# Kernel tuning notes

Measured on AMD Instinct MI355X. Metric: run time of the kernel, lower is better.

Reference implementation:

```python
import jax, jax.numpy as jnp
import numpy as np

N_HEADS = 4
DIM_K = 64
DIM_V = 64
D_MODEL = 256


def setup_inputs() -> dict:
    key = jax.random.key(0)
    ks = jax.random.split(key, 10)
    B, S = 8, 1024
    s = 1.0 / np.sqrt(D_MODEL)
    return {
        "x": jax.random.normal(ks[0], (B, S, D_MODEL), jnp.float32),
        "y": jax.random.normal(ks[1], (B, S, D_MODEL), jnp.float32),
        "Wq": jax.random.normal(ks[2], (D_MODEL, DIM_K * N_HEADS), jnp.float32) * s,
        "bq": jnp.zeros((DIM_K * N_HEADS,), jnp.float32),
        "Wk": jax.random.normal(ks[3], (D_MODEL, DIM_K * N_HEADS), jnp.float32) * s,
        "bk": jnp.zeros((DIM_K * N_HEADS,), jnp.float32),
        "Wv": jax.random.normal(ks[4], (D_MODEL, DIM_V * N_HEADS), jnp.float32) * s,
        "bv": jnp.zeros((DIM_V * N_HEADS,), jnp.float32),
        "Wo": jax.random.normal(ks[5], (DIM_V * N_HEADS, D_MODEL), jnp.float32) * s,
        "bo": jnp.zeros((D_MODEL,), jnp.float32),
    }


def reference(x, y, Wq, bq, Wk, bk, Wv, bv, Wo, bo):
    B, Sx, _ = x.shape
    Sy = y.shape[1]
    dk = DIM_K // N_HEADS  # head dim for Q/K (16)
    dv = DIM_V // N_HEADS  # head dim for V (16)
    # Faithful to the original reshape: leading dim becomes n_heads^2 pseudo-heads.
    Q = (x @ Wq + bq).reshape(-1, B, Sx, dk)   # [H2, B, Sx, dk]
    K = (y @ Wk + bk).reshape(-1, B, Sy, dk)   # [H2, B, Sy, dk]
    V = (y @ Wv + bv).reshape(-1, B, Sy, dv)   # [H2, B, Sy, dv]
    scale = 1.0 / np.sqrt(DIM_K)
    scores = jnp.einsum("hbqd,hbkd->hbqk", Q, K) * scale  # [H2, B, Sx, Sy]
    # Per-row lower median (torch.median semantics: lower of two middle values).
    n = scores.shape[-1]
    med = jnp.sort(scores, axis=-1)[..., (n - 1) // 2][..., None]
    # Mask out entries not strictly greater than the row median.
    scores = jnp.where(scores - med > 0, scores, -jnp.inf)
    probs = jax.nn.softmax(scores, axis=-1)
    out = jnp.einsum("hbqk,hbkd->hbqd", probs, V)          # [H2, B, Sx, dv]
    out = jnp.transpose(out, (0, 2, 1, 3)).reshape(B, Sx, -1)  # [B, Sx, H2*dv]
    return out @ Wo + bo
```

## Files before the change

kernel.cpp:

```cpp
#include <hip/hip_runtime.h>
#include <stdint.h>


typedef _Float16 f16x8 __attribute__((ext_vector_type(8)));
typedef _Float16 f16x4 __attribute__((ext_vector_type(4)));
typedef float    f32x4 __attribute__((ext_vector_type(4)));

__global__ __launch_bounds__(256) void prepW(
    const float* __restrict__ Wq, const float* __restrict__ Wk,
    const float* __restrict__ Wv, const float* __restrict__ Wo,
    _Float16* __restrict__ P)
{
    __shared__ float T[64][65];
    const int mat = blockIdx.y;
    const float* W = (mat == 0) ? Wq : (mat == 1) ? Wk : (mat == 2) ? Wv : Wo;
    const int tk = blockIdx.x >> 2, tn = blockIdx.x & 3;
    const int t  = threadIdx.x;
    const int cl = t & 63, rg = t >> 6;

    #pragma unroll
    for (int r = 0; r < 16; ++r) {
        const int k = (rg << 4) + r;
        T[k][cl] = W[(size_t)((tk << 6) + k) * 256 + (tn << 6) + cl];
    }
    __syncthreads();
    _Float16* hi = P + ((size_t)mat << 17);
    _Float16* lo = hi + 65536;
    #pragma unroll
    for (int r = 0; r < 16; ++r) {
        const int n = (rg << 4) + r;
        const float v = T[cl][n];
        const _Float16 h = (_Float16)v;
        const size_t o = (size_t)((tn << 6) + n) * 256 + (tk << 6) + cl;
        hi[o] = h;
        lo[o] = (_Float16)(v - (float)h);
    }
}

__device__ __forceinline__ void gemm_mfma(const float* __restrict__ A,
                                          const _Float16* __restrict__ Whi,
                                          const _Float16* __restrict__ Wlo,
                                          const float* __restrict__ bias,
                                          float* __restrict__ C, int vf16)
{
    __shared__ _Float16 Bhi[64][136];
    __shared__ _Float16 Blo[64][136];
    const int tid = threadIdx.x;
    const int m0 = blockIdx.x << 7, n0 = blockIdx.y << 6;

    const int wv = tid >> 6, lane = tid & 63;
    const int fm = lane & 15, fq = lane >> 4;
    const int arow = m0 + (wv << 4) + fm;
    const float* abase = A + (size_t)arow * 256;

    const int srow = tid >> 4;
    const int skl  = (tid & 15) << 3;

    f32x4 acc[4];
    #pragma unroll
    for (int cb = 0; cb < 4; ++cb) { acc[cb][0]=0.f; acc[cb][1]=0.f; acc[cb][2]=0.f; acc[cb][3]=0.f; }

    float4 a0 = *(const float4*)(abase + (fq << 3));
    float4 a1 = *(const float4*)(abase + (fq << 3) + 4);

    #pragma unroll
    for (int h = 0; h < 2; ++h) {
        if (h) __syncthreads();
        #pragma unroll
        for (int p = 0; p < 2; ++p) {
            const int n = (p << 5) + srow;
            const size_t off = (size_t)(n0 + n) * 256 + (h << 7) + skl;
            *(f16x8*)&Bhi[n][skl] = *(const f16x8*)(Whi + off);
            *(f16x8*)&Blo[n][skl] = *(const f16x8*)(Wlo + off);
        }
        __syncthreads();

        #pragma unroll
        for (int kb = 0; kb < 4; ++kb) {
            const int ks = (h << 2) + kb;
            float4 n0v = a0, n1v = a1;
            if (ks < 7) {
                const float* np = abase + ((ks + 1) << 5) + (fq << 3);
                n0v = *(const float4*)np;
                n1v = *(const float4*)(np + 4);
            }
            const float ae[8] = {a0.x, a0.y, a0.z, a0.w, a1.x, a1.y, a1.z, a1.w};
            f16x8 Ah, Al;
            #pragma unroll
            for (int j = 0; j < 8; ++j) {
                const _Float16 hh = (_Float16)ae[j];
                Ah[j] = hh;
                Al[j] = (_Float16)(ae[j] - (float)hh);
            }
            #pragma unroll
            for (int cb = 0; cb < 4; ++cb) {
                f16x8 Bh = *(const f16x8*)&Bhi[(cb << 4) + fm][(kb << 5) + (fq << 3)];
                f16x8 Bl = *(const f16x8*)&Blo[(cb << 4) + fm][(kb << 5) + (fq << 3)];
                acc[cb] = __builtin_amdgcn_mfma_f32_16x16x32_f16(Ah, Bh, acc[cb], 0, 0, 0);
                acc[cb] = __builtin_amdgcn_mfma_f32_16x16x32_f16(Al, Bh, acc[cb], 0, 0, 0);
                acc[cb] = __builtin_amdgcn_mfma_f32_16x16x32_f16(Ah, Bl, acc[cb], 0, 0, 0);
            }
            a0 = n0v; a1 = n1v;
        }
    }

    if (vf16) {
        _Float16* Cv = (_Float16*)C;
        #pragma unroll
        for (int cb = 0; cb < 4; ++cb) {
            const float bb = bias[n0 + (cb << 4) + fm];
            #pragma unroll
            for (int i = 0; i < 4; ++i)
                Cv[(size_t)(m0 + (wv << 4) + (fq << 2) + i) * 256
                   + n0 + (cb << 4) + fm] = (_Float16)(acc[cb][i] + bb);
        }
    } else {
        #pragma unroll
        for (int cb = 0; cb < 4; ++cb) {
            const float bb = bias[n0 + (cb << 4) + fm];
            #pragma unroll
            for (int i = 0; i < 4; ++i)
                C[(size_t)(m0 + (wv << 4) + (fq << 2) + i) * 256
                  + n0 + (cb << 4) + fm] = acc[cb][i] + bb;
        }
    }
}

__global__ __attribute__((amdgpu_waves_per_eu(6, 6)))
__launch_bounds__(512) void gemmQKV(
    const float* __restrict__ x, const float* __restrict__ y,
    const _Float16* __restrict__ WP,
    const float* __restrict__ bq, const float* __restrict__ bk,
    const float* __restrict__ bv,
    float* __restrict__ Q, float* __restrict__ K, float* __restrict__ Vf)
{
    const int z = blockIdx.z;
    const float* A = (z == 0) ? x  : y;
    const _Float16* Whi = WP + ((size_t)z << 17);
    const _Float16* Wlo = Whi + 65536;
    const float* b = (z == 0) ? bq : (z == 1) ? bk : bv;
    float*       C = (z == 0) ? Q  : (z == 1) ? K  : Vf;
    gemm_mfma(A, Whi, Wlo, b, C, z == 2);
}

__global__ __attribute__((amdgpu_waves_per_eu(6, 6)))
__launch_bounds__(512) void gemmOut(
    const float* __restrict__ A, const _Float16* __restrict__ WP,
    const float* __restrict__ b, float* __restrict__ C)
{
    const _Float16* Whi = WP + ((size_t)3 << 17);
    const _Float16* Wlo = Whi + 65536;
    gemm_mfma(A, Whi, Wlo, b, C, 0);
}

__device__ __forceinline__ float u2f(unsigned int m) {
    unsigned int x = (m & 0x80000000u) ? (m ^ 0x80000000u) : ~m;
    return __uint_as_float(x);
}
__device__ __forceinline__ unsigned int f2u(float f) {
    unsigned int x = __float_as_uint(f);
    return (x & 0x80000000u) ? ~x : (x | 0x80000000u);
}

__device__ __forceinline__ float wred_sum(float x) {
    x += __int_as_float(__builtin_amdgcn_update_dpp(0, __float_as_int(x), 0x111, 0xF, 0xF, true));
    x += __int_as_float(__builtin_amdgcn_update_dpp(0, __float_as_int(x), 0x112, 0xF, 0xF, true));
    x += __int_as_float(__builtin_amdgcn_update_dpp(0, __float_as_int(x), 0x114, 0xF, 0xF, true));
    x += __int_as_float(__builtin_amdgcn_update_dpp(0, __float_as_int(x), 0x118, 0xF, 0xF, true));
    x += __int_as_float(__builtin_amdgcn_update_dpp(0, __float_as_int(x), 0x142, 0xF, 0xF, true));
    x += __int_as_float(__builtin_amdgcn_update_dpp(0, __float_as_int(x), 0x143, 0xF, 0xF, true));
    return __int_as_float(__builtin_amdgcn_readlane(__float_as_int(x), 63));
}
__device__ __forceinline__ float wred_min(float x) {
    const int IDENT = 0x7f7fffff;
    x = fminf(x, __int_as_float(__builtin_amdgcn_update_dpp(IDENT, __float_as_int(x), 0x111, 0xF, 0xF, false)));
    x = fminf(x, __int_as_float(__builtin_amdgcn_update_dpp(IDENT, __float_as_int(x), 0x112, 0xF, 0xF, false)));
    x = fminf(x, __int_as_float(__builtin_amdgcn_update_dpp(IDENT, __float_as_int(x), 0x114, 0xF, 0xF, false)));
    x = fminf(x, __int_as_float(__builtin_amdgcn_update_dpp(IDENT, __float_as_int(x), 0x118, 0xF, 0xF, false)));
    x = fminf(x, __int_as_float(__builtin_amdgcn_update_dpp(IDENT, __float_as_int(x), 0x142, 0xF, 0xF, false)));
    x = fminf(x, __int_as_float(__builtin_amdgcn_update_dpp(IDENT, __float_as_int(x), 0x143, 0xF, 0xF, false)));
    return __int_as_float(__builtin_amdgcn_readlane(__float_as_int(x), 63));
}
__device__ __forceinline__ float wred_max(float x) {
    const int IDENT = (int)0xff7fffff;
    x = fmaxf(x, __int_as_float(__builtin_amdgcn_update_dpp(IDENT, __float_as_int(x), 0x111, 0xF, 0xF, false)));
    x = fmaxf(x, __int_as_float(__builtin_amdgcn_update_dpp(IDENT, __float_as_int(x), 0x112, 0xF, 0xF, false)));
    x = fmaxf(x, __int_as_float(__builtin_amdgcn_update_dpp(IDENT, __float_as_int(x), 0x114, 0xF, 0xF, false)));
    x = fmaxf(x, __int_as_float(__builtin_amdgcn_update_dpp(IDENT, __float_as_int(x), 0x118, 0xF, 0xF, false)));
    x = fmaxf(x, __int_as_float(__builtin_amdgcn_update_dpp(IDENT, __float_as_int(x), 0x142, 0xF, 0xF, false)));
    x = fmaxf(x, __int_as_float(__builtin_amdgcn_update_dpp(IDENT, __float_as_int(x), 0x143, 0xF, 0xF, false)));
    return __int_as_float(__builtin_amdgcn_readlane(__float_as_int(x), 63));
}

__global__ __attribute__((amdgpu_waves_per_eu(6, 6)))
__launch_bounds__(512) void attn(
    const float* __restrict__ Qb, const float* __restrict__ Kb,
    const _Float16* __restrict__ Vb, float* __restrict__ Ob)
{
    __shared__ union {
        float    Ssc[8][1028];
        _Float16 Vt[16][1032];
    } U;
    __shared__ float part[1024];
    __shared__ float sums[2][8];

    const int tid  = threadIdx.x;
    const int wave = tid >> 6, lane = tid & 63;
    const int head = blockIdx.x, grp = blockIdx.y;
    const float*    Qh = Qb + ((size_t)head << 14);
    const float*    Kh = Kb + ((size_t)head << 14);
    const _Float16* Vh = Vb + ((size_t)head << 14);
    const int fm = lane & 15, fq = lane >> 4;

    for (int i = tid; i < 4096; i += 512) {
        f16x4 v = ((const f16x4*)Vh)[i];
        const int k = i >> 2, d0 = (i & 3) << 2;
        U.Vt[d0 + 0][k] = v[0];
        U.Vt[d0 + 1][k] = v[1];
        U.Vt[d0 + 2][k] = v[2];
        U.Vt[d0 + 3][k] = v[3];
    }
    __syncthreads();
    f16x8 Vf[4];
    #pragma unroll
    for (int kb = 0; kb < 4; ++kb)
        Vf[kb] = *(const f16x8*)&U.Vt[fm][(((wave << 2) + kb) << 5) + (fq << 3)];

    f16x8 Bp[8];
    #pragma unroll
    for (int kb = 0; kb < 8; ++kb) {
        const int krow = (wave << 7) + (kb << 4) + fm;
        float4 kv = *(const float4*)(Kh + ((size_t)krow << 4) + (fq << 2));
        const float ke[4] = {kv.x * 0.125f, kv.y * 0.125f,
                             kv.z * 0.125f, kv.w * 0.125f};
        #pragma unroll
        for (int j = 0; j < 4; ++j) {
            _Float16 h = (_Float16)ke[j];
            Bp[kb][j]     = h;
            Bp[kb][j + 4] = (_Float16)(ke[j] - (float)h);
        }
    }
    __syncthreads();

    const int cstart = (grp * 128) / 6;
    const int cend   = ((grp + 1) * 128) / 6;

    for (int chunk = cstart; chunk < cend; ++chunk) {
        const int qbase = chunk << 3;
        const int sb = chunk & 1;

        f16x8 A1, A2;
        {
            const int arow = qbase + (fm & 7);
            float4 qv = *(const float4*)(Qh + ((size_t)arow << 4) + (fq << 2));
            const float qe[4] = {qv.x, qv.y, qv.z, qv.w};
            #pragma unroll
            for (int j = 0; j < 4; ++j) {
                _Float16 h = (_Float16)qe[j];
                A1[j] = h; A1[j + 4] = h;
                A2[j] = (_Float16)(qe[j] - (float)h);
                A2[j + 4] = (_Float16)0.f;
            }
        }
        #pragma unroll
        for (int kb = 0; kb < 8; ++kb) {
            f32x4 c = {0.f, 0.f, 0.f, 0.f};
            c = __builtin_amdgcn_mfma_f32_16x16x32_f16(A1, Bp[kb], c, 0, 0, 0);
            c = __builtin_amdgcn_mfma_f32_16x16x32_f16(A2, Bp[kb], c, 0, 0, 0);
            if (fq < 2) {
                const int col = (wave << 7) + (kb << 4) + fm;
                #pragma unroll
                for (int i = 0; i < 4; ++i)
                    U.Ssc[(fq << 2) + i][col] = c[i];
            }
        }
        __syncthreads();

        float s[16];
        #pragma unroll
        for (int b = 0; b < 4; ++b) {
            f32x4 v = *(const f32x4*)&U.Ssc[wave][(b << 8) + (lane << 2)];
            s[(b << 2) + 0] = v.x; s[(b << 2) + 1] = v.y;
            s[(b << 2) + 2] = v.z; s[(b << 2) + 3] = v.w;
        }

        float mn = 0.f, sq = 0.f;
        #pragma unroll
        for (int j = 0; j < 16; ++j) { mn += s[j]; sq += s[j] * s[j]; }
        mn = wred_sum(mn);
        sq = wred_sum(sq);
        mn *= (1.0f / 1024.0f);
        const float var  = fmaxf(sq * (1.0f / 1024.0f) - mn * mn, 1e-12f);
        const float step = __builtin_sqrtf(var) * 0.0024479f;

        unsigned int lo = 0x00800000u, hi = 0xFF7FFFFFu;
        int cl = 0, ch = 1024;
        float vL = -3.4e38f, vH = 3.4e38f;
        float t = mn, medf = 0.f;
        int found = 0;
        for (int pass = 0; pass < 64 && !found; ++pass) {
            int cnt = 0;
            #pragma unroll
            for (int j = 0; j < 16; ++j)
                cnt += __popcll(__ballot(s[j] <= t));
            const unsigned int tc = f2u(t);
            if (cnt >= 512) { hi = tc; ch = cnt; vH = t; }
            else            { lo = tc + 1; cl = cnt; vL = t; }

            if (cl == 511) {
                float c = 3.4e38f;
                #pragma unroll
                for (int j = 0; j < 16; ++j)
                    c = fminf(c, (s[j] > vL) ? s[j] : 3.4e38f);
                medf = wred_min(c); found = 1;
            } else if (ch == 512) {
                float c = -3.4e38f;
                #pragma unroll
                for (int j = 0; j < 16; ++j)
                    c = fmaxf(c, (s[j] <= vH) ? s[j] : -3.4e38f);
                medf = wred_max(c); found = 1;
            } else if (cl == 510) {
                float m1 = 3.4e38f;
                #pragma unroll
                for (int j = 0; j < 16; ++j)
                    m1 = fminf(m1, (s[j] > vL) ? s[j] : 3.4e38f);
                m1 = wred_min(m1);
                int c1 = 0;
                #pragma unroll
                for (int j = 0; j < 16; ++j)
                    c1 += __popcll(__ballot(s[j] <= m1));
                if (c1 >= 512) { medf = m1; }
                else {
                    float c2 = 3.4e38f;
                    #pragma unroll
                    for (int j = 0; j < 16; ++j)
                        c2 = fminf(c2, (s[j] > m1) ? s[j] : 3.4e38f);
                    medf = wred_min(c2);
                }
                found = 1;
            } else if (ch == 513) {
                float m1 = -3.4e38f;
                #pragma unroll
                for (int j = 0; j < 16; ++j)
                    m1 = fmaxf(m1, (s[j] <= vH) ? s[j] : -3.4e38f);
                m1 = wred_max(m1);
                int c1 = 0;
                #pragma unroll
                for (int j = 0; j < 16; ++j)
                    c1 += __popcll(__ballot(s[j] < m1));
                if (c1 <= 511) { medf = m1; }
                else {
                    float c2 = -3.4e38f;
                    #pragma unroll
                    for (int j = 0; j < 16; ++j)
                        c2 = fmaxf(c2, (s[j] < m1) ? s[j] : -3.4e38f);
                    medf = wred_max(c2);
                }
                found = 1;
            } else if (lo >= hi) {
                medf = u2f(lo); found = 1;
            } else {
                float tn = t + (511.5f - (float)cnt) * step;
                bool ok = (tn > vL) && (tn < vH);
                if (pass >= 5 && (pass & 1)) ok = false;
                t = ok ? tn : u2f(lo + ((hi - lo) >> 1));
            }
        }
        if (!found) medf = u2f(lo);

        _Float16* Pw = (_Float16*)&U.Ssc[wave][0];
        float sum = 0.f;
        #pragma unroll
        for (int b = 0; b < 4; ++b) {
            f16x4 hv;
            #pragma unroll
            for (int jj = 0; jj < 4; ++jj) {
                float e = (s[(b << 2) + jj] > medf) ? __expf(s[(b << 2) + jj]) : 0.f;
                _Float16 h = (_Float16)e;
                hv[jj] = h;
                sum += (float)h;
            }
            *(f16x4*)&Pw[(b << 8) + (lane << 2)] = hv;
        }
        sum = wred_sum(sum);
        if (lane == 0) sums[sb][wave] = sum;
        __syncthreads();

        f32x4 acc = {0.f, 0.f, 0.f, 0.f};
        const _Float16* Pr = (const _Float16*)&U.Ssc[fm & 7][0] + (fq << 3);
        #pragma unroll
        for (int kb = 0; kb < 4; ++kb) {
            f16x8 a = *(const f16x8*)(Pr + ((((wave << 2) + kb)) << 5));
            acc = __builtin_amdgcn_mfma_f32_16x16x32_f16(a, Vf[kb], acc, 0, 0, 0);
        }
        if (lane < 32) {
            #pragma unroll
            for (int i = 0; i < 4; ++i)
                part[(wave << 7) + (((fq << 2) + i) << 4) + fm] = acc[i];
        }
        __syncthreads();

        const int rw = (wave - chunk) & 7;
        if (rw < 2) {
            const int t2 = (rw << 6) + lane;
            const int r = t2 >> 4, d = t2 & 15;
            float o = 0.f;
            #pragma unroll
            for (int w = 0; w < 8; ++w) o += part[(w << 7) + t2];
            const float inv = 1.0f / sums[sb][r];
            const int q = qbase + r;
            const int h = head >> 3, bp = head & 7;
            float* dst = Ob + (((size_t)(h >> 1)) << 18)
                            + ((size_t)(((h & 1) << 9) + (q >> 1)) << 8)
                            + ((q & 1) << 7) + (bp << 4) + d;
            *dst = o * inv;
        }
    }
}

extern "C" void kernel_launch(void* const* d_in, const int* in_sizes, int n_in,
                              void* d_out, int out_size, void* d_ws, size_t ws_size,
                              hipStream_t stream) {
    const float* x  = (const float*)d_in[0];
    const float* y  = (const float*)d_in[1];
    const float* Wq = (const float*)d_in[2];
    const float* bq = (const float*)d_in[3];
    const float* Wk = (const float*)d_in[4];
    const float* bk = (const float*)d_in[5];
    const float* Wv = (const float*)d_in[6];
    const float* bv = (const float*)d_in[7];
    const float* Wo = (const float*)d_in[8];
    const float* bo = (const float*)d_in[9];
    float* out = (float*)d_out;

    float*     Q  = (float*)d_ws;
    float*     K  = Q + 2097152;
    _Float16*  V  = (_Float16*)(K + 2097152);
    float*     AO = (float*)d_ws + 5242880;
    _Float16*  WP = (_Float16*)((float*)d_ws + 7340032);

    prepW<<<dim3(16, 4), dim3(256), 0, stream>>>(Wq, Wk, Wv, Wo, WP);
    gemmQKV<<<dim3(64, 4, 3), dim3(512), 0, stream>>>(x, y, WP, bq, bk, bv,
                                                      Q, K, (float*)V);
    attn<<<dim3(128, 6), dim3(512), 0, stream>>>(Q, K, V, AO);
    gemmOut<<<dim3(64, 4), dim3(512), 0, stream>>>(AO, WP, bo, out);
}
```

Baseline: 270.9 us.

## Double-buffer attention scratch to drop a barrier per chunk and regrid

Double-buffers the score/probability scratch, the partial-output buffer and the row sums by chunk parity. The cross-wave reduction and output write for each chunk are deferred into the next iteration, which removes one __syncthreads per chunk, and a final epilogue handles the last chunk. Grid changes from 128x6 to 128x4 with 32 chunks per block. The waves_per_eu hint drops from 6 to 4, since LDS use roughly doubles and limits occupancy.

Result: slower. 291.6 us (+7.6%).

```diff
diff --git a/kernel.cpp b/kernel.cpp
--- a/kernel.cpp
+++ b/kernel.cpp
@@ -192,16 +192,16 @@
     return __int_as_float(__builtin_amdgcn_readlane(__float_as_int(x), 63));
 }
 
-__global__ __attribute__((amdgpu_waves_per_eu(6, 6)))
+__global__ __attribute__((amdgpu_waves_per_eu(4, 4)))
 __launch_bounds__(512) void attn(
     const float* __restrict__ Qb, const float* __restrict__ Kb,
     const _Float16* __restrict__ Vb, float* __restrict__ Ob)
 {
     __shared__ union {
-        float    Ssc[8][1028];
+        float    Ssc[2][8][1028];
         _Float16 Vt[16][1032];
     } U;
-    __shared__ float part[1024];
+    __shared__ float part[2][1024];
     __shared__ float sums[2][8];
 
     const int tid  = threadIdx.x;
@@ -242,12 +242,12 @@
     }
     __syncthreads();
 
-    const int cstart = (grp * 128) / 6;
-    const int cend   = ((grp + 1) * 128) / 6;
+    const int cstart = grp << 5;
+    const int cend   = cstart + 32;
 
     for (int chunk = cstart; chunk < cend; ++chunk) {
         const int qbase = chunk << 3;
-        const int sb = chunk & 1;
+        const int p = chunk & 1;
 
         f16x8 A1, A2;
         {
@@ -271,7 +271,7 @@
                 const int col = (wave << 7) + (kb << 4) + fm;
                 #pragma unroll
                 for (int i = 0; i < 4; ++i)
-                    U.Ssc[(fq << 2) + i][col] = c[i];
+                    U.Ssc[p][(fq << 2) + i][col] = c[i];
             }
         }
         __syncthreads();
@@ -279,7 +279,7 @@
         float s[16];
         #pragma unroll
         for (int b = 0; b < 4; ++b) {
-            f32x4 v = *(const f32x4*)&U.Ssc[wave][(b << 8) + (lane << 2)];
+            f32x4 v = *(const f32x4*)&U.Ssc[p][wave][(b << 8) + (lane << 2)];
             s[(b << 2) + 0] = v.x; s[(b << 2) + 1] = v.y;
             s[(b << 2) + 2] = v.z; s[(b << 2) + 3] = v.w;
         }
@@ -368,7 +368,7 @@
         }
         if (!found) medf = u2f(lo);
 
-        _Float16* Pw = (_Float16*)&U.Ssc[wave][0];
+        _Float16* Pw = (_Float16*)&U.Ssc[p][wave][0];
         float sum = 0.f;
         #pragma unroll
         for (int b = 0; b < 4; ++b) {
@@ -383,11 +383,11 @@
             *(f16x4*)&Pw[(b << 8) + (lane << 2)] = hv;
         }
         sum = wred_sum(sum);
-        if (lane == 0) sums[sb][wave] = sum;
+        if (lane == 0) sums[p][wave] = sum;
         __syncthreads();
 
         f32x4 acc = {0.f, 0.f, 0.f, 0.f};
-        const _Float16* Pr = (const _Float16*)&U.Ssc[fm & 7][0] + (fq << 3);
+        const _Float16* Pr = (const _Float16*)&U.Ssc[p][fm & 7][0] + (fq << 3);
         #pragma unroll
         for (int kb = 0; kb < 4; ++kb) {
             f16x8 a = *(const f16x8*)(Pr + ((((wave << 2) + kb)) << 5));
@@ -396,19 +396,41 @@
         if (lane < 32) {
             #pragma unroll
             for (int i = 0; i < 4; ++i)
-                part[(wave << 7) + (((fq << 2) + i) << 4) + fm] = acc[i];
-        }
-        __syncthreads();
-
-        const int rw = (wave - chunk) & 7;
+                part[p][(wave << 7) + (((fq << 2) + i) << 4) + fm] = acc[i];
+        }
+
+        if (chunk > cstart) {
+            const int pc = chunk - 1, pp = p ^ 1;
+            const int rw = (wave - pc) & 7;
+            if (rw < 2) {
+                const int t2 = (rw << 6) + lane;
+                const int r = t2 >> 4, d = t2 & 15;
+                float o = 0.f;
+                #pragma unroll
+                for (int w = 0; w < 8; ++w) o += part[pp][(w << 7) + t2];
+                const float inv = 1.0f / sums[pp][r];
+                const int q = (pc << 3) + r;
+                const int h = head >> 3, bp = head & 7;
+                float* dst = Ob + (((size_t)(h >> 1)) << 18)
+                                + ((size_t)(((h & 1) << 9) + (q >> 1)) << 8)
+                                + ((q & 1) << 7) + (bp << 4) + d;
+                *dst = o * inv;
+            }
+        }
+    }
+
+    __syncthreads();
+    {
+        const int pc = cend - 1, pp = pc & 1;
+        const int rw = (wave - pc) & 7;
         if (rw < 2) {
             const int t2 = (rw << 6) + lane;
             const int r = t2 >> 4, d = t2 & 15;
             float o = 0.f;
             #pragma unroll
-            for (int w = 0; w < 8; ++w) o += part[(w << 7) + t2];
-            const float inv = 1.0f / sums[sb][r];
-            const int q = qbase + r;
+            for (int w = 0; w < 8; ++w) o += part[pp][(w << 7) + t2];
+            const float inv = 1.0f / sums[pp][r];
+            const int q = (pc << 3) + r;
             const int h = head >> 3, bp = head & 7;
             float* dst = Ob + (((size_t)(h >> 1)) << 18)
                             + ((size_t)(((h & 1) << 9) + (q >> 1)) << 8)
@@ -442,6 +464,6 @@
     prepW<<<dim3(16, 4), dim3(256), 0, stream>>>(Wq, Wk, Wv, Wo, WP);
     gemmQKV<<<dim3(64, 4, 3), dim3(512), 0, stream>>>(x, y, WP, bq, bk, bv,
                                                       Q, K, (float*)V);
-    attn<<<dim3(128, 6), dim3(512), 0, stream>>>(Q, K, V, AO);
+    attn<<<dim3(128, 4), dim3(512), 0, stream>>>(Q, K, V, AO);
     gemmOut<<<dim3(64, 4), dim3(512), 0, stream>>>(AO, WP, bo, out);
 }
```

## Write V pre-transposed from QKV GEMM and load V fragments from global in attention

Applied to the files above, without the earlier changes.

The QKV GEMM epilogue now writes V in a per-head transposed layout, packing four half values per store. The attention kernel no longer stages and transposes V through shared memory at startup, so the union, the transpose loop and one barrier go away. V fragments are instead loaded directly from global memory inside the chunk loop on every iteration, which relies on cache hits and adds global loads per chunk.

Measured after the change: 260.4 us. 3.9% less time.

```diff
diff --git a/kernel.cpp b/kernel.cpp
--- a/kernel.cpp
+++ b/kernel.cpp
@@ -105,14 +105,20 @@
     }
 
     if (vf16) {
-        _Float16* Cv = (_Float16*)C;
-        #pragma unroll
-        for (int cb = 0; cb < 4; ++cb) {
-            const float bb = bias[n0 + (cb << 4) + fm];
-            #pragma unroll
-            for (int i = 0; i < 4; ++i)
-                Cv[(size_t)(m0 + (wv << 4) + (fq << 2) + i) * 256
-                   + n0 + (cb << 4) + fm] = (_Float16)(acc[cb][i] + bb);
+        _Float16* Vt = (_Float16*)C;
+        float bb[4];
+        #pragma unroll
+        for (int cb = 0; cb < 4; ++cb) bb[cb] = bias[n0 + (cb << 4) + fm];
+        #pragma unroll
+        for (int i = 0; i < 4; ++i) {
+            const int m = m0 + (wv << 4) + (fq << 2) + i;
+            f16x4 v;
+            #pragma unroll
+            for (int cb = 0; cb < 4; ++cb)
+                v[cb] = (_Float16)(acc[cb][i] + bb[cb]);
+            const size_t o = ((size_t)(m >> 6) << 14) + ((size_t)fm << 10)
+                           + ((m & 63) << 4) + (n0 >> 4);
+            *(f16x4*)&Vt[o] = v;
         }
     } else {
         #pragma unroll
@@ -197,10 +203,7 @@
     const float* __restrict__ Qb, const float* __restrict__ Kb,
     const _Float16* __restrict__ Vb, float* __restrict__ Ob)
 {
-    __shared__ union {
-        float    Ssc[8][1028];
-        _Float16 Vt[16][1032];
-    } U;
+    __shared__ float Ssc[8][1028];
     __shared__ float part[1024];
     __shared__ float sums[2][8];
 
@@ -212,20 +215,6 @@
     const _Float16* Vh = Vb + ((size_t)head << 14);
     const int fm = lane & 15, fq = lane >> 4;
 
-    for (int i = tid; i < 4096; i += 512) {
-        f16x4 v = ((const f16x4*)Vh)[i];
-        const int k = i >> 2, d0 = (i & 3) << 2;
-        U.Vt[d0 + 0][k] = v[0];
-        U.Vt[d0 + 1][k] = v[1];
-        U.Vt[d0 + 2][k] = v[2];
-        U.Vt[d0 + 3][k] = v[3];
-    }
-    __syncthreads();
-    f16x8 Vf[4];
-    #pragma unroll
-    for (int kb = 0; kb < 4; ++kb)
-        Vf[kb] = *(const f16x8*)&U.Vt[fm][(((wave << 2) + kb) << 5) + (fq << 3)];
-
     f16x8 Bp[8];
     #pragma unroll
     for (int kb = 0; kb < 8; ++kb) {
@@ -240,7 +229,7 @@
             Bp[kb][j + 4] = (_Float16)(ke[j] - (float)h);
         }
     }
-    __syncthreads();
+    const _Float16* vfb = Vh + ((size_t)fm << 10) + (wave << 7) + (fq << 3);
 
     const int cstart = (grp * 128) / 6;
     const int cend   = ((grp + 1) * 128) / 6;
@@ -271,7 +260,7 @@
                 const int col = (wave << 7) + (kb << 4) + fm;
                 #pragma unroll
                 for (int i = 0; i < 4; ++i)
-                    U.Ssc[(fq << 2) + i][col] = c[i];
+                    Ssc[(fq << 2) + i][col] = c[i];
             }
         }
         __syncthreads();
@@ -279,7 +268,7 @@
         float s[16];
         #pragma unroll
         for (int b = 0; b < 4; ++b) {
-            f32x4 v = *(const f32x4*)&U.Ssc[wave][(b << 8) + (lane << 2)];
+            f32x4 v = *(const f32x4*)&Ssc[wave][(b << 8) + (lane << 2)];
             s[(b << 2) + 0] = v.x; s[(b << 2) + 1] = v.y;
             s[(b << 2) + 2] = v.z; s[(b << 2) + 3] = v.w;
         }
@@ -368,7 +357,7 @@
         }
         if (!found) medf = u2f(lo);
 
-        _Float16* Pw = (_Float16*)&U.Ssc[wave][0];
+        _Float16* Pw = (_Float16*)&Ssc[wave][0];
         float sum = 0.f;
         #pragma unroll
         for (int b = 0; b < 4; ++b) {
@@ -387,11 +376,12 @@
         __syncthreads();
 
         f32x4 acc = {0.f, 0.f, 0.f, 0.f};
-        const _Float16* Pr = (const _Float16*)&U.Ssc[fm & 7][0] + (fq << 3);
+        const _Float16* Pr = (const _Float16*)&Ssc[fm & 7][0] + (fq << 3);
         #pragma unroll
         for (int kb = 0; kb < 4; ++kb) {
+            f16x8 vf = *(const f16x8*)(vfb + (kb << 5));
             f16x8 a = *(const f16x8*)(Pr + ((((wave << 2) + kb)) << 5));
-            acc = __builtin_amdgcn_mfma_f32_16x16x32_f16(a, Vf[kb], acc, 0, 0, 0);
+            acc = __builtin_amdgcn_mfma_f32_16x16x32_f16(a, vf, acc, 0, 0, 0);
         }
         if (lane < 32) {
             #pragma unroll
@@ -435,13 +425,13 @@
 
     float*     Q  = (float*)d_ws;
     float*     K  = Q + 2097152;
-    _Float16*  V  = (_Float16*)(K + 2097152);
+    _Float16*  VT = (_Float16*)(K + 2097152);
     float*     AO = (float*)d_ws + 5242880;
     _Float16*  WP = (_Float16*)((float*)d_ws + 7340032);
 
     prepW<<<dim3(16, 4), dim3(256), 0, stream>>>(Wq, Wk, Wv, Wo, WP);
     gemmQKV<<<dim3(64, 4, 3), dim3(512), 0, stream>>>(x, y, WP, bq, bk, bv,
-                                                      Q, K, (float*)V);
-    attn<<<dim3(128, 6), dim3(512), 0, stream>>>(Q, K, V, AO);
+                                                      Q, K, (float*)VT);
+    attn<<<dim3(128, 6), dim3(512), 0, stream>>>(Q, K, VT, AO);
     gemmOut<<<dim3(64, 4), dim3(512), 0, stream>>>(AO, WP, bo, out);
 }
```
